# Kernel optimization log

Measured on AMD Instinct MI355X. Metric: run time of the kernel, lower is better.

The kernel has to match this reference:

```python
import jax, jax.numpy as jnp
import numpy as np

# DCRNN (PEMS-BAY scale) constants
N = 325      # num_nodes
B = 64       # batch_size
T = 12       # encoder seq_len
HZ = 12      # decoder horizon
U = 64       # rnn_units
DIN = 2      # input_dim
DOUT = 1     # output_dim
K = 2        # max_diffusion_step
NM = K + 1   # num diffusion matrices (Chebyshev, single laplacian support)


def _glorot(key, shape):
    lim = float(np.sqrt(6.0 / (shape[0] + shape[1])))
    return jax.random.uniform(key, shape, jnp.float32, -lim, lim)


def setup_inputs() -> dict:
    key = jax.random.key(0)
    ks = jax.random.split(key, 8)
    # random symmetric adjacency -> scaled Laplacian support (lambda_max ~= 2 approx)
    a = np.asarray(jax.random.uniform(ks[0], (N, N)))
    a = (a + a.T) * 0.5
    a = a * (a > 0.9)
    d = a.sum(1)
    dinv = 1.0 / np.sqrt(np.maximum(d, 1e-8))
    L = np.eye(N, dtype=np.float32) - (dinv[:, None] * a * dinv[None, :]).astype(np.float32)
    support = jnp.asarray(L - np.eye(N, dtype=np.float32))  # 2L/lambda_max - I with lambda_max=2

    def cell_params(k, din):
        f = (din + U) * NM
        k1, k2 = jax.random.split(k)
        return dict(gate_W=_glorot(k1, (f, 2 * U)), gate_b=jnp.zeros((2 * U,), jnp.float32),
                    cand_W=_glorot(k2, (f, U)), cand_b=jnp.zeros((U,), jnp.float32))

    inp = {"inputs": jax.random.normal(ks[1], (T, B, N * DIN), jnp.float32),
           "support": support}
    for name, din, kk in [("enc0", DIN, ks[2]), ("enc1", U, ks[3]),
                          ("dec0", DOUT, ks[4]), ("dec1", U, ks[5])]:
        for pn, v in cell_params(kk, din).items():
            inp[f"{name}_{pn}"] = v
    inp["proj_W"] = _glorot(ks[6], (U, DOUT))
    inp["proj_b"] = jnp.zeros((DOUT,), jnp.float32)
    return inp


def _gconv(x, support, W, b):
    # x: (B, N, F). Chebyshev diffusion: x0=x, x1=Lx, x2=2Lx1-x0, ...
    xs = [x]
    x0, x1 = x, jnp.einsum('mn,bnf->bmf', support, x)
    xs.append(x1)
    for _ in range(2, K + 1):
        x2 = 2.0 * jnp.einsum('mn,bnf->bmf', support, x1) - x0
        xs.append(x2)
        x0, x1 = x1, x2
    xk = jnp.concatenate(xs, axis=-1)  # (B, N, NM*F)
    return xk @ W + b


def _gru_cell(x, h, support, gW, gb, cW, cb):
    # diffusion-conv GRU: r,u gates then candidate
    ru = jax.nn.sigmoid(_gconv(jnp.concatenate([x, h], -1), support, gW, gb))
    r, u = jnp.split(ru, 2, axis=-1)
    c = jnp.tanh(_gconv(jnp.concatenate([x, r * h], -1), support, cW, cb))
    return u * h + (1.0 - u) * c


def reference(inputs, support,
              enc0_gate_W, enc0_gate_b, enc0_cand_W, enc0_cand_b,
              enc1_gate_W, enc1_gate_b, enc1_cand_W, enc1_cand_b,
              dec0_gate_W, dec0_gate_b, dec0_cand_W, dec0_cand_b,
              dec1_gate_W, dec1_gate_b, dec1_cand_W, dec1_cand_b,
              proj_W, proj_b):
    x_seq = inputs.reshape(T, B, N, DIN)
    h0 = jnp.zeros((B, N, U), inputs.dtype)

    def enc_step(carry, x):
        h_l0, h_l1 = carry
        h_l0 = _gru_cell(x, h_l0, support, enc0_gate_W, enc0_gate_b, enc0_cand_W, enc0_cand_b)
        h_l1 = _gru_cell(h_l0, h_l1, support, enc1_gate_W, enc1_gate_b, enc1_cand_W, enc1_cand_b)
        return (h_l0, h_l1), None

    (h_l0, h_l1), _ = jax.lax.scan(enc_step, (h0, h0), x_seq)

    def dec_step(carry, _):
        d_in, hd0, hd1 = carry
        hd0 = _gru_cell(d_in, hd0, support, dec0_gate_W, dec0_gate_b, dec0_cand_W, dec0_cand_b)
        hd1 = _gru_cell(hd0, hd1, support, dec1_gate_W, dec1_gate_b, dec1_cand_W, dec1_cand_b)
        out = hd1 @ proj_W + proj_b  # (B, N, DOUT)
        return (out, hd0, hd1), out.reshape(B, N * DOUT)

    start = jnp.zeros((B, N, DOUT), inputs.dtype)  # GO symbol
    _, outputs = jax.lax.scan(dec_step, (start, h_l0, h_l1), None, length=HZ)
    return outputs  # (horizon, B, N*DOUT)
```

## Files before the change

### kernel.cpp

```cpp
#include <hip/hip_runtime.h>

constexpr int N  = 325;
constexpr int B  = 64;
constexpr int T  = 12;
constexpr int HZ = 12;
constexpr int U  = 64;
constexpr int BN = B * N;

constexpr int SSTIL = 42;
constexpr int SSKC  = 11;
constexpr int XST   = 364;

typedef __attribute__((ext_vector_type(8))) short short8;
typedef __attribute__((ext_vector_type(4))) float floatx4;

__device__ inline unsigned short f2bf(float f) {
    unsigned u = __float_as_uint(f);
    u += 0x7fff + ((u >> 16) & 1);
    return (unsigned short)(u >> 16);
}
__device__ inline unsigned pack_hilo(float v) {
    const unsigned short hi = f2bf(v);
    const float hif = __uint_as_float(((unsigned)hi) << 16);
    const unsigned short lo = f2bf(v - hif);
    return (unsigned)hi | ((unsigned)lo << 16);
}
__device__ inline void unpack8(const uint4 u0, const uint4 u1,
                               short8& h, short8& l) {
    const unsigned uu[8] = {u0.x, u0.y, u0.z, u0.w, u1.x, u1.y, u1.z, u1.w};
    #pragma unroll
    for (int j = 0; j < 8; ++j) {
        h[j] = (short)(uu[j] & 0xffffu);
        l[j] = (short)(uu[j] >> 16);
    }
}


__global__ void zero_kernel(unsigned* __restrict__ p, long n) {
    long i = (long)blockIdx.x * blockDim.x + threadIdx.x;
    const long stride = (long)gridDim.x * blockDim.x;
    for (; i < n; i += stride) p[i] = 0u;
}

__global__ __launch_bounds__(256)
void s2_build(const float* __restrict__ S, float* __restrict__ S2)
{
    const int m = blockIdx.x;
    __shared__ float srow[N];
    for (int i = threadIdx.x; i < N; i += 256) srow[i] = S[m * N + i];
    __syncthreads();
    for (int c = threadIdx.x; c < N; c += 256) {
        float a = 0.f;
        for (int k = 0; k < N; ++k) a += srow[k] * S[k * N + c];
        S2[m * N + c] = a;
    }
}

__global__ __launch_bounds__(64)
void prepack_ss(const float* __restrict__ S, const float* __restrict__ S2,
                short* __restrict__ ssh, short* __restrict__ ssl)
{
    const int t = blockIdx.x, kc = blockIdx.y, lane = threadIdx.x;
    const int quad = lane >> 4, l15 = lane & 15;
    short8 hv, lv;
    #pragma unroll
    for (int j = 0; j < 8; ++j) {
        const int m = t * 16 + l15;
        const int k = kc * 32 + quad * 8 + j;
        float v = 0.f;
        if (k < N) {
            if (m < N) v = S[m * N + k];
            else if (m >= 336 && m < 336 + N) v = S2[(m - 336) * N + k];
        }
        const unsigned short hb = f2bf(v);
        hv[j] = (short)hb;
        lv[j] = (short)f2bf(v - __uint_as_float(((unsigned)hb) << 16));
    }
    const size_t off = ((size_t)(t * SSKC + kc) * 64 + lane);
    ((short8*)ssh)[off] = hv;
    ((short8*)ssl)[off] = lv;
}

__global__ __launch_bounds__(64)
void prepack_w(const float* __restrict__ W, short* __restrict__ Wh,
               short* __restrict__ Wl, int F, int Nout, int NT, int Z0KC)
{
    const int kc = blockIdx.x, n = blockIdx.y, lane = threadIdx.x;
    const int quad = lane >> 4, l15 = lane & 15;
    short8 hv, lv;
    #pragma unroll
    for (int j = 0; j < 8; ++j) {
        const int p   = kc * 32 + quad * 8 + j;
        const int col = n * 16 + l15;
        float w = 0.f;
        if (p < Z0KC * 32) {
            const int f = p;
            if (f < F)
                w = W[(size_t)f * Nout + col] - W[(size_t)(2 * F + f) * Nout + col];
        } else {
            const int q = p - Z0KC * 32;
            if (q < F)
                w = W[(size_t)(F + q) * Nout + col];
            else if (q < 2 * F)
                w = 2.f * W[(size_t)(2 * F + (q - F)) * Nout + col];
        }
        const unsigned short hb = f2bf(w);
        hv[j] = (short)hb;
        lv[j] = (short)f2bf(w - __uint_as_float(((unsigned)hb) << 16));
    }
    const size_t off = ((size_t)(kc * NT + n) * 64 + lane);
    ((short8*)Wh)[off] = hv;
    ((short8*)Wl)[off] = lv;
}

template<int DIN, int F, bool RM, bool ZV>
__device__ __forceinline__ void z0_frag(const float* __restrict__ x,
    const float* __restrict__ h, const float* __restrict__ ru,
    int row, int kc, int quad, short8& ah, short8& al)
{
    float v[8];
    if constexpr (ZV) {
        const int k0 = kc * 32 + quad * 8;
        if (k0 < 64) {
            const float4 a = *(const float4*)&x[(size_t)row * 64 + k0];
            const float4 b = *(const float4*)&x[(size_t)row * 64 + k0 + 4];
            v[0]=a.x; v[1]=a.y; v[2]=a.z; v[3]=a.w;
            v[4]=b.x; v[5]=b.y; v[6]=b.z; v[7]=b.w;
        } else {
            const int kk = k0 - 64;
            float4 a = *(const float4*)&h[(size_t)row * 64 + kk];
            float4 b = *(const float4*)&h[(size_t)row * 64 + kk + 4];
            if constexpr (RM) {
                const float4 ra = *(const float4*)&ru[(size_t)row * 128 + kk];
                const float4 rb = *(const float4*)&ru[(size_t)row * 128 + kk + 4];
                a.x *= ra.x; a.y *= ra.y; a.z *= ra.z; a.w *= ra.w;
                b.x *= rb.x; b.y *= rb.y; b.z *= rb.z; b.w *= rb.w;
            }
            v[0]=a.x; v[1]=a.y; v[2]=a.z; v[3]=a.w;
            v[4]=b.x; v[5]=b.y; v[6]=b.z; v[7]=b.w;
        }
    } else {
        #pragma unroll
        for (int j = 0; j < 8; ++j) {
            const int k = kc * 32 + quad * 8 + j;
            float t = 0.f;
            if (k < DIN) t = x[(size_t)row * DIN + k];
            else if (k < F) {
                t = h[(size_t)row * 64 + (k - DIN)];
                if constexpr (RM) t *= ru[(size_t)row * 128 + (k - DIN)];
            }
            v[j] = t;
        }
    }
    #pragma unroll
    for (int j = 0; j < 8; ++j) {
        const unsigned u = pack_hilo(v[j]);
        ah[j] = (short)(u & 0xffffu);
        al[j] = (short)(u >> 16);
    }
}

template<int DIN, int F, int YP, bool RMUL, bool VEC>
__device__ __forceinline__ void diffuse_body(
    const short8* __restrict__ ssh, const short8* __restrict__ ssl,
    const float* __restrict__ x, const float* __restrict__ h,
    const float* __restrict__ ru, unsigned* __restrict__ zcat,
    int cx, int b, unsigned* __restrict__ xls)
{
    const int c0 = cx * 32;
    const int tid = threadIdx.x, wave = tid >> 6, lane = tid & 63;
    const int quad = lane >> 4, l15 = lane & 15;

    if constexpr (VEC) {
        for (int idx4 = tid; idx4 < 352 * 8; idx4 += 896) {
            const int n = idx4 >> 3, f = (idx4 & 7) * 4, gf = c0 + f;
            uint4 pk = make_uint4(0u, 0u, 0u, 0u);
            if (n < N) {
                const int row = b * N + n;
                float4 v;
                if (gf < DIN) {
                    v = *(const float4*)&x[(size_t)row * DIN + gf];
                } else {
                    v = *(const float4*)&h[(size_t)row * U + (gf - DIN)];
                    if (RMUL) {
                        const float4 rv = *(const float4*)&ru[(size_t)row * 128 + (gf - DIN)];
                        v.x *= rv.x; v.y *= rv.y; v.z *= rv.z; v.w *= rv.w;
                    }
                }
                pk.x = pack_hilo(v.x); pk.y = pack_hilo(v.y);
                pk.z = pack_hilo(v.z); pk.w = pack_hilo(v.w);
            }
            xls[(f + 0) * XST + n] = pk.x;
            xls[(f + 1) * XST + n] = pk.y;
            xls[(f + 2) * XST + n] = pk.z;
            xls[(f + 3) * XST + n] = pk.w;
        }
    } else {
        for (int idx = tid; idx < 352 * 32; idx += 896) {
            const int n = idx >> 5, f = idx & 31, gf = c0 + f;
            unsigned u = 0u;
            if (n < N && gf < F) {
                const int row = b * N + n;
                float v;
                if (gf < DIN) {
                    v = x[(size_t)row * DIN + gf];
                } else {
                    v = h[(size_t)row * U + (gf - DIN)];
                    if (RMUL) v *= ru[(size_t)row * 128 + (gf - DIN)];
                }
                u = pack_hilo(v);
            }
            xls[f * XST + n] = u;
        }
    }
    __syncthreads();

    const int tb = wave * 3;

    floatx4 acc[3][2];
    #pragma unroll
    for (int i = 0; i < 3; ++i)
        #pragma unroll
        for (int n = 0; n < 2; ++n)
            acc[i][n] = (floatx4){0.f, 0.f, 0.f, 0.f};

    short8 cah[3], cal[3], nah[3], nal[3];
    #pragma unroll
    for (int i = 0; i < 3; ++i) {
        const size_t fo = (size_t)((tb + i) * SSKC) * 64 + lane;
        cah[i] = ssh[fo]; cal[i] = ssl[fo];
    }
    for (int kc = 0; kc < SSKC; ++kc) {
        if (kc + 1 < SSKC) {
            #pragma unroll
            for (int i = 0; i < 3; ++i) {
                const size_t fo = (size_t)((tb + i) * SSKC + kc + 1) * 64 + lane;
                nah[i] = ssh[fo]; nal[i] = ssl[fo];
            }
        }
        short8 bh[2], bl[2];
        const int koff = kc * 32 + quad * 8;
        #pragma unroll
        for (int n = 0; n < 2; ++n) {
            const uint4 u0 = *(const uint4*)&xls[(n * 16 + l15) * XST + koff];
            const uint4 u1 = *(const uint4*)&xls[(n * 16 + l15) * XST + koff + 4];
            unpack8(u0, u1, bh[n], bl[n]);
        }
        #pragma unroll
        for (int i = 0; i < 3; ++i)
            #pragma unroll
            for (int n = 0; n < 2; ++n) {
                acc[i][n] = __builtin_amdgcn_mfma_f32_16x16x32_bf16(cah[i], bh[n], acc[i][n], 0, 0, 0);
                acc[i][n] = __builtin_amdgcn_mfma_f32_16x16x32_bf16(cah[i], bl[n], acc[i][n], 0, 0, 0);
                acc[i][n] = __builtin_amdgcn_mfma_f32_16x16x32_bf16(cal[i], bh[n], acc[i][n], 0, 0, 0);
            }
        if (kc + 1 < SSKC) {
            #pragma unroll
            for (int i = 0; i < 3; ++i) { cah[i] = nah[i]; cal[i] = nal[i]; }
        }
    }

    #pragma unroll
    for (int i = 0; i < 3; ++i) {
        const int t = tb + i;
        #pragma unroll
        for (int n = 0; n < 2; ++n) {
            const int col = c0 + n * 16 + l15;
            if (col >= F) continue;
            #pragma unroll
            for (int r = 0; r < 4; ++r) {
                const int m = t * 16 + quad * 4 + r;
                if (m < N)
                    zcat[(size_t)(b * N + m) * YP + col] = pack_hilo(acc[i][n][r]);
                else if (m >= 336 && m < 336 + N)
                    zcat[(size_t)(b * N + (m - 336)) * YP + F + col] = pack_hilo(acc[i][n][r]);
            }
        }
    }
}


template<int DIN, int F, int Z0KC, int YKC, bool ZV>
__device__ __forceinline__ void gate_body(const unsigned* __restrict__ zcat,
    const float* __restrict__ x, const float* __restrict__ h,
    const short8* __restrict__ Wh, const short8* __restrict__ Wl,
    const float* __restrict__ bias, float* __restrict__ ruout, int bx, int nb)
{
    constexpr int YP = YKC * 32, NT = 4;
    const int tid = threadIdx.x, wave = tid >> 6, lane = tid & 63;
    const int quad = lane >> 4, l15 = lane & 15;
    const int row0 = bx * 64 + wave * 16;
    const int row = row0 + l15;

    floatx4 acc[NT];
    #pragma unroll
    for (int n = 0; n < NT; ++n) {
        const float bv = bias[(nb + n) * 16 + l15];
        acc[n] = (floatx4){bv, bv, bv, bv};
    }
    for (int kc = 0; kc < Z0KC; ++kc) {
        short8 ahi, alo;
        z0_frag<DIN, F, false, ZV>(x, h, nullptr, row, kc, quad, ahi, alo);
        const short8* __restrict__ wh = Wh + (size_t)(kc * 8 + nb) * 64 + lane;
        const short8* __restrict__ wl = Wl + (size_t)(kc * 8 + nb) * 64 + lane;
        #pragma unroll
        for (int n = 0; n < NT; ++n) {
            const short8 bh = wh[n * 64], bl = wl[n * 64];
            acc[n] = __builtin_amdgcn_mfma_f32_16x16x32_bf16(ahi, bh, acc[n], 0, 0, 0);
            acc[n] = __builtin_amdgcn_mfma_f32_16x16x32_bf16(ahi, bl, acc[n], 0, 0, 0);
            acc[n] = __builtin_amdgcn_mfma_f32_16x16x32_bf16(alo, bh, acc[n], 0, 0, 0);
        }
    }
    const unsigned* __restrict__ zrow = zcat + (size_t)row * YP + quad * 8;
    for (int kc = 0; kc < YKC; ++kc) {
        const uint4* p = (const uint4*)(zrow + kc * 32);
        short8 ahi, alo;
        unpack8(p[0], p[1], ahi, alo);
        const short8* __restrict__ wh = Wh + (size_t)((Z0KC + kc) * 8 + nb) * 64 + lane;
        const short8* __restrict__ wl = Wl + (size_t)((Z0KC + kc) * 8 + nb) * 64 + lane;
        #pragma unroll
        for (int n = 0; n < NT; ++n) {
            const short8 bh = wh[n * 64], bl = wl[n * 64];
            acc[n] = __builtin_amdgcn_mfma_f32_16x16x32_bf16(ahi, bh, acc[n], 0, 0, 0);
            acc[n] = __builtin_amdgcn_mfma_f32_16x16x32_bf16(ahi, bl, acc[n], 0, 0, 0);
            acc[n] = __builtin_amdgcn_mfma_f32_16x16x32_bf16(alo, bh, acc[n], 0, 0, 0);
        }
    }
    #pragma unroll
    for (int n = 0; n < NT; ++n) {
        const int col = (nb + n) * 16 + l15;
        #pragma unroll
        for (int r = 0; r < 4; ++r) {
            const int rw = row0 + quad * 4 + r;
            ruout[(size_t)rw * 128 + col] = 1.f / (1.f + __expf(-acc[n][r]));
        }
    }
}

template<int DIN, int F, int Z0KC, int YKC, bool ZV>
__device__ __forceinline__ void cand_body(const unsigned* __restrict__ zcat,
    const float* __restrict__ x, const float* __restrict__ h,
    const float* __restrict__ ru, const short8* __restrict__ Wh,
    const short8* __restrict__ Wl, const float* __restrict__ bias,
    float* __restrict__ hout, int bx, int nb)
{
    constexpr int YP = YKC * 32, NT = 2;
    const int tid = threadIdx.x, wave = tid >> 6, lane = tid & 63;
    const int quad = lane >> 4, l15 = lane & 15;
    const int row0 = bx * 64 + wave * 16;
    const int row = row0 + l15;

    floatx4 acc[NT];
    #pragma unroll
    for (int n = 0; n < NT; ++n) {
        const float bv = bias[(nb + n) * 16 + l15];
        acc[n] = (floatx4){bv, bv, bv, bv};
    }
    for (int kc = 0; kc < Z0KC; ++kc) {
        short8 ahi, alo;
        z0_frag<DIN, F, true, ZV>(x, h, ru, row, kc, quad, ahi, alo);
        const short8* __restrict__ wh = Wh + (size_t)(kc * 4 + nb) * 64 + lane;
        const short8* __restrict__ wl = Wl + (size_t)(kc * 4 + nb) * 64 + lane;
        #pragma unroll
        for (int n = 0; n < NT; ++n) {
            const short8 bh = wh[n * 64], bl = wl[n * 64];
            acc[n] = __builtin_amdgcn_mfma_f32_16x16x32_bf16(ahi, bh, acc[n], 0, 0, 0);
            acc[n] = __builtin_amdgcn_mfma_f32_16x16x32_bf16(ahi, bl, acc[n], 0, 0, 0);
            acc[n] = __builtin_amdgcn_mfma_f32_16x16x32_bf16(alo, bh, acc[n], 0, 0, 0);
        }
    }
    const unsigned* __restrict__ zrow = zcat + (size_t)row * YP + quad * 8;
    for (int kc = 0; kc < YKC; ++kc) {
        const uint4* p = (const uint4*)(zrow + kc * 32);
        short8 ahi, alo;
        unpack8(p[0], p[1], ahi, alo);
        const short8* __restrict__ wh = Wh + (size_t)((Z0KC + kc) * 4 + nb) * 64 + lane;
        const short8* __restrict__ wl = Wl + (size_t)((Z0KC + kc) * 4 + nb) * 64 + lane;
        #pragma unroll
        for (int n = 0; n < NT; ++n) {
            const short8 bh = wh[n * 64], bl = wl[n * 64];
            acc[n] = __builtin_amdgcn_mfma_f32_16x16x32_bf16(ahi, bh, acc[n], 0, 0, 0);
            acc[n] = __builtin_amdgcn_mfma_f32_16x16x32_bf16(ahi, bl, acc[n], 0, 0, 0);
            acc[n] = __builtin_amdgcn_mfma_f32_16x16x32_bf16(alo, bh, acc[n], 0, 0, 0);
        }
    }
    #pragma unroll
    for (int n = 0; n < NT; ++n) {
        const int col = (nb + n) * 16 + l15;
        #pragma unroll
        for (int r = 0; r < 4; ++r) {
            const int rw = row0 + quad * 4 + r;
            const float c  = tanhf(acc[n][r]);
            const float ug = ru[(size_t)rw * 128 + 64 + col];
            const float hv = h[(size_t)rw * 64 + col];
            hout[(size_t)rw * 64 + col] = ug * hv + (1.f - ug) * c;
        }
    }
}


template<int DIN, int F, int YP, bool RMUL, int CB, bool VEC>
__global__ __launch_bounds__(896, 7)
void diffuse_solo(const short8* __restrict__ ssh, const short8* __restrict__ ssl,
                  const float* __restrict__ x, const float* __restrict__ h,
                  const float* __restrict__ ru, unsigned* __restrict__ zcat)
{
    __shared__ __align__(16) unsigned xls[32 * XST];
    diffuse_body<DIN, F, YP, RMUL, VEC>(ssh, ssl, x, h, ru, zcat,
                                        CB + blockIdx.x, blockIdx.y, xls);
}

template<int DIN, int F, int Z0KC, int YKC, bool ZV>
__global__ __launch_bounds__(256)
void gate_cell(const unsigned* __restrict__ zcat, const float* __restrict__ x,
               const float* __restrict__ h, const short8* __restrict__ Wh,
               const short8* __restrict__ Wl, const float* __restrict__ bias,
               float* __restrict__ ru)
{
    gate_body<DIN, F, Z0KC, YKC, ZV>(zcat, x, h, Wh, Wl, bias, ru,
                                     blockIdx.x, blockIdx.y * 4);
}

template<int DIN, int F, int Z0KC, int YKC, bool ZV>
__global__ __launch_bounds__(256)
void cand_cell(const unsigned* __restrict__ zcat, const float* __restrict__ x,
               const float* __restrict__ h, const float* __restrict__ ru,
               const short8* __restrict__ Wh, const short8* __restrict__ Wl,
               const float* __restrict__ bias, float* __restrict__ hout)
{
    cand_body<DIN, F, Z0KC, YKC, ZV>(zcat, x, h, ru, Wh, Wl, bias, hout,
                                     blockIdx.x, blockIdx.y * 2);
}

__global__ __launch_bounds__(256)
void cand_proj(const unsigned* __restrict__ zcat, const float* __restrict__ x,
               const float* __restrict__ h, const float* __restrict__ ru,
               const short8* __restrict__ Wh, const short8* __restrict__ Wl,
               const float* __restrict__ bias, float* __restrict__ hout,
               const float* __restrict__ pW, const float* __restrict__ pb,
               float* __restrict__ outp, float* __restrict__ dec_in)
{
    constexpr int Z0KC = 4, YKC = 8, YP = 256, NT = 4;
    const int tid = threadIdx.x, wave = tid >> 6, lane = tid & 63;
    const int quad = lane >> 4, l15 = lane & 15;
    const int row0 = blockIdx.x * 64 + wave * 16;
    const int row = row0 + l15;

    floatx4 acc[NT];
    #pragma unroll
    for (int n = 0; n < NT; ++n) {
        const float bv = bias[n * 16 + l15];
        acc[n] = (floatx4){bv, bv, bv, bv};
    }
    for (int kc = 0; kc < Z0KC; ++kc) {
        short8 ahi, alo;
        z0_frag<64, 128, true, true>(x, h, ru, row, kc, quad, ahi, alo);
        const short8* __restrict__ wh = Wh + (size_t)(kc * 4) * 64 + lane;
        const short8* __restrict__ wl = Wl + (size_t)(kc * 4) * 64 + lane;
        #pragma unroll
        for (int n = 0; n < NT; ++n) {
            const short8 bh = wh[n * 64], bl = wl[n * 64];
            acc[n] = __builtin_amdgcn_mfma_f32_16x16x32_bf16(ahi, bh, acc[n], 0, 0, 0);
            acc[n] = __builtin_amdgcn_mfma_f32_16x16x32_bf16(ahi, bl, acc[n], 0, 0, 0);
            acc[n] = __builtin_amdgcn_mfma_f32_16x16x32_bf16(alo, bh, acc[n], 0, 0, 0);
        }
    }
    const unsigned* __restrict__ zrow = zcat + (size_t)row * YP + quad * 8;
    for (int kc = 0; kc < YKC; ++kc) {
        const uint4* p = (const uint4*)(zrow + kc * 32);
        short8 ahi, alo;
        unpack8(p[0], p[1], ahi, alo);
        const short8* __restrict__ wh = Wh + (size_t)((Z0KC + kc) * 4) * 64 + lane;
        const short8* __restrict__ wl = Wl + (size_t)((Z0KC + kc) * 4) * 64 + lane;
        #pragma unroll
        for (int n = 0; n < NT; ++n) {
            const short8 bh = wh[n * 64], bl = wl[n * 64];
            acc[n] = __builtin_amdgcn_mfma_f32_16x16x32_bf16(ahi, bh, acc[n], 0, 0, 0);
            acc[n] = __builtin_amdgcn_mfma_f32_16x16x32_bf16(ahi, bl, acc[n], 0, 0, 0);
            acc[n] = __builtin_amdgcn_mfma_f32_16x16x32_bf16(alo, bh, acc[n], 0, 0, 0);
        }
    }
    float pr[4] = {0.f, 0.f, 0.f, 0.f};
    #pragma unroll
    for (int n = 0; n < NT; ++n) {
        const int col = n * 16 + l15;
        const float pw = pW[col];
        #pragma unroll
        for (int r = 0; r < 4; ++r) {
            const int rw = row0 + quad * 4 + r;
            const float c  = tanhf(acc[n][r]);
            const float ug = ru[(size_t)rw * 128 + 64 + col];
            const float hv = h[(size_t)rw * 64 + col];
            const float hn = ug * hv + (1.f - ug) * c;
            hout[(size_t)rw * 64 + col] = hn;
            pr[r] += hn * pw;
        }
    }
    #pragma unroll
    for (int r = 0; r < 4; ++r) {
        float v = pr[r];
        v += __shfl_xor(v, 1); v += __shfl_xor(v, 2);
        v += __shfl_xor(v, 4); v += __shfl_xor(v, 8);
        if (l15 == 0) {
            const int rw = row0 + quad * 4 + r;
            const float o = v + pb[0];
            outp[rw]   = o;
            dec_in[rw] = o;
        }
    }
}


struct DuoDP {
    const short8 *ssh, *ssl;
    const float *xA, *hA, *ruA; unsigned* zA;
    const float *xB, *hB, *ruB; unsigned* zB;
    int cA, cbB;
};

template<bool RM>
__global__ __launch_bounds__(896, 7)
void diffuse_duo(DuoDP P)
{
    __shared__ __align__(16) unsigned xls[32 * XST];
    if ((int)blockIdx.x < P.cA)
        diffuse_body<2, 66, 160, RM, false>(P.ssh, P.ssl, P.xA, P.hA, P.ruA,
                                            P.zA, blockIdx.x, blockIdx.y, xls);
    else
        diffuse_body<64, 128, 256, RM, true>(P.ssh, P.ssl, P.xB, P.hB, P.ruB,
                                             P.zB, P.cbB + blockIdx.x - P.cA,
                                             blockIdx.y, xls);
}

struct DuoGP {
    const unsigned* zA; const float *xA, *hA;
    const short8 *WhA, *WlA; const float* bA; float* ruA;
    const unsigned* zB; const float *xB, *hB;
    const short8 *WhB, *WlB; const float* bB; float* ruB;
};

__global__ __launch_bounds__(256)
void gate_duo(DuoGP P)
{
    if (blockIdx.z == 0)
        gate_body<2, 66, 3, 5, false>(P.zA, P.xA, P.hA, P.WhA, P.WlA, P.bA,
                                      P.ruA, blockIdx.x, blockIdx.y * 4);
    else
        gate_body<64, 128, 4, 8, true>(P.zB, P.xB, P.hB, P.WhB, P.WlB, P.bB,
                                       P.ruB, blockIdx.x, blockIdx.y * 4);
}

struct DuoCP {
    const unsigned* zA; const float *xA, *hA, *ruA;
    const short8 *WhA, *WlA; const float* bA; float* hoA;
    const unsigned* zB; const float *xB, *hB, *ruB;
    const short8 *WhB, *WlB; const float* bB; float* hoB;
};

__global__ __launch_bounds__(256)
void cand_duo(DuoCP P)
{
    if (blockIdx.z == 0)
        cand_body<2, 66, 3, 5, false>(P.zA, P.xA, P.hA, P.ruA, P.WhA, P.WlA,
                                      P.bA, P.hoA, blockIdx.x, blockIdx.y * 2);
    else
        cand_body<64, 128, 4, 8, true>(P.zB, P.xB, P.hB, P.ruB, P.WhB, P.WlB,
                                       P.bB, P.hoB, blockIdx.x, blockIdx.y * 2);
}


extern "C" void kernel_launch(void* const* d_in, const int* in_sizes, int n_in,
                              void* d_out, int out_size, void* d_ws, size_t ws_size,
                              hipStream_t stream)
{
    const float* inputs = (const float*)d_in[0];
    const float* S      = (const float*)d_in[1];
    const float* Wt[4][4];
    for (int l = 0; l < 4; ++l)
        for (int j = 0; j < 4; ++j)
            Wt[l][j] = (const float*)d_in[2 + l * 4 + j];
    const float* pW = (const float*)d_in[18];
    const float* pb = (const float*)d_in[19];
    float* out = (float*)d_out;

    float*    ws     = (float*)d_ws;
    float*    H0[2]  = {ws, ws + (size_t)BN * U};
    float*    H1[2]  = {ws + 2 * (size_t)BN * U, ws + 3 * (size_t)BN * U};
    float*    dec_in = ws + 4 * (size_t)BN * U;
    float*    ruA    = dec_in + BN;
    float*    ruB    = ruA + (size_t)BN * 128;
    unsigned* zcatA  = (unsigned*)(ruB + (size_t)BN * 128);
    unsigned* zcatB  = zcatA + (size_t)BN * 160;
    float*    S2     = (float*)(zcatB + (size_t)BN * 256);
    char*     pp     = (char*)(S2 + (size_t)N * N);
    pp = (char*)(((uintptr_t)pp + 15) & ~(uintptr_t)15);

    short* ssh = (short*)pp;
    short* ssl = ssh + (size_t)SSTIL * SSKC * 64 * 8;
    char*  wpbase = (char*)(ssl + (size_t)SSTIL * SSKC * 64 * 8);

    const int Fs[4]   = {66, 128, 65, 128};
    const int KPs[4]  = {256, 384, 256, 384};
    const int Z0s[4]  = {3, 4, 3, 4};
    short *Wgh[4], *Wgl[4], *Wch[4], *Wcl[4];
    size_t off = 0;
    for (int l = 0; l < 4; ++l) {
        const size_t ge = (size_t)KPs[l] * 128, ce = (size_t)KPs[l] * 64;
        Wgh[l] = (short*)(wpbase + off); off += ge * 2;
        Wgl[l] = (short*)(wpbase + off); off += ge * 2;
        Wch[l] = (short*)(wpbase + off); off += ce * 2;
        Wcl[l] = (short*)(wpbase + off); off += ce * 2;
    }

    const long zn = (long)BN * (4 * U) + BN + (long)BN * 256 + (long)BN * (160 + 256);
    zero_kernel<<<2048, 256, 0, stream>>>((unsigned*)ws, zn);

    s2_build<<<N, 256, 0, stream>>>(S, S2);
    prepack_ss<<<dim3(SSTIL, SSKC), 64, 0, stream>>>(S, S2, ssh, ssl);
    for (int l = 0; l < 4; ++l) {
        prepack_w<<<dim3(KPs[l] / 32, 8), 64, 0, stream>>>(Wt[l][0], Wgh[l], Wgl[l],
                                                           Fs[l], 128, 8, Z0s[l]);
        prepack_w<<<dim3(KPs[l] / 32, 4), 64, 0, stream>>>(Wt[l][2], Wch[l], Wcl[l],
                                                           Fs[l], 64, 4, Z0s[l]);
    }

    const short8* SSH = (const short8*)ssh;
    const short8* SSL = (const short8*)ssl;
    int p0 = 0, p1 = 0;

    for (int s = 0; s <= T; ++s) {
        const float* x0 = inputs + (size_t)s * BN * 2;
        const bool a = (s < T), b1 = (s >= 1);
        if (a && b1) {
            DuoDP dp{SSH, SSL, x0, H0[p0], nullptr, zcatA,
                     H0[p0], H1[p1], nullptr, zcatB, 3, 0};
            diffuse_duo<false><<<dim3(7, B), 896, 0, stream>>>(dp);
            DuoGP gp{zcatA, x0, H0[p0], (short8*)Wgh[0], (short8*)Wgl[0], Wt[0][1], ruA,
                     zcatB, H0[p0], H1[p1], (short8*)Wgh[1], (short8*)Wgl[1], Wt[1][1], ruB};
            gate_duo<<<dim3(BN / 64, 2, 2), 256, 0, stream>>>(gp);
            DuoDP dp2{SSH, SSL, x0, H0[p0], ruA, zcatA,
                      H0[p0], H1[p1], ruB, zcatB, 3, 2};
            diffuse_duo<true><<<dim3(5, B), 896, 0, stream>>>(dp2);
            DuoCP cp{zcatA, x0, H0[p0], ruA, (short8*)Wch[0], (short8*)Wcl[0], Wt[0][3], H0[p0 ^ 1],
                     zcatB, H0[p0], H1[p1], ruB, (short8*)Wch[1], (short8*)Wcl[1], Wt[1][3], H1[p1 ^ 1]};
            cand_duo<<<dim3(BN / 64, 2, 2), 256, 0, stream>>>(cp);
            p0 ^= 1; p1 ^= 1;
        } else if (a) {
            diffuse_solo<2, 66, 160, false, 0, false><<<dim3(3, B), 896, 0, stream>>>(
                SSH, SSL, x0, H0[p0], nullptr, zcatA);
            gate_cell<2, 66, 3, 5, false><<<dim3(BN / 64, 2), 256, 0, stream>>>(
                zcatA, x0, H0[p0], (short8*)Wgh[0], (short8*)Wgl[0], Wt[0][1], ruA);
            diffuse_solo<2, 66, 160, true, 0, false><<<dim3(3, B), 896, 0, stream>>>(
                SSH, SSL, x0, H0[p0], ruA, zcatA);
            cand_cell<2, 66, 3, 5, false><<<dim3(BN / 64, 2), 256, 0, stream>>>(
                zcatA, x0, H0[p0], ruA, (short8*)Wch[0], (short8*)Wcl[0], Wt[0][3], H0[p0 ^ 1]);
            p0 ^= 1;
        } else {
            diffuse_solo<64, 128, 256, false, 0, true><<<dim3(4, B), 896, 0, stream>>>(
                SSH, SSL, H0[p0], H1[p1], nullptr, zcatB);
            gate_cell<64, 128, 4, 8, true><<<dim3(BN / 64, 2), 256, 0, stream>>>(
                zcatB, H0[p0], H1[p1], (short8*)Wgh[1], (short8*)Wgl[1], Wt[1][1], ruB);
            diffuse_solo<64, 128, 256, true, 2, true><<<dim3(2, B), 896, 0, stream>>>(
                SSH, SSL, H0[p0], H1[p1], ruB, zcatB);
            cand_cell<64, 128, 4, 8, true><<<dim3(BN / 64, 2), 256, 0, stream>>>(
                zcatB, H0[p0], H1[p1], ruB, (short8*)Wch[1], (short8*)Wcl[1], Wt[1][3], H1[p1 ^ 1]);
            p1 ^= 1;
        }
    }

    for (int hz = 0; hz < HZ; ++hz) {
        diffuse_solo<1, 65, 160, false, 0, false><<<dim3(3, B), 896, 0, stream>>>(
            SSH, SSL, dec_in, H0[p0], nullptr, zcatB);
        gate_cell<1, 65, 3, 5, false><<<dim3(BN / 64, 2), 256, 0, stream>>>(
            zcatB, dec_in, H0[p0], (short8*)Wgh[2], (short8*)Wgl[2], Wt[2][1], ruA);
        diffuse_solo<1, 65, 160, true, 0, false><<<dim3(3, B), 896, 0, stream>>>(
            SSH, SSL, dec_in, H0[p0], ruA, zcatB);
        cand_cell<1, 65, 3, 5, false><<<dim3(BN / 64, 2), 256, 0, stream>>>(
            zcatB, dec_in, H0[p0], ruA, (short8*)Wch[2], (short8*)Wcl[2], Wt[2][3], H0[p0 ^ 1]);
        p0 ^= 1;
        diffuse_solo<64, 128, 256, false, 0, true><<<dim3(4, B), 896, 0, stream>>>(
            SSH, SSL, H0[p0], H1[p1], nullptr, zcatB);
        gate_cell<64, 128, 4, 8, true><<<dim3(BN / 64, 2), 256, 0, stream>>>(
            zcatB, H0[p0], H1[p1], (short8*)Wgh[3], (short8*)Wgl[3], Wt[3][1], ruA);
        diffuse_solo<64, 128, 256, true, 2, true><<<dim3(2, B), 896, 0, stream>>>(
            SSH, SSL, H0[p0], H1[p1], ruA, zcatB);
        cand_proj<<<BN / 64, 256, 0, stream>>>(
            zcatB, H0[p0], H1[p1], ruA, (short8*)Wch[3], (short8*)Wcl[3], Wt[3][3],
            H1[p1 ^ 1], pW, pb, out + (size_t)hz * BN, dec_in);
        p1 ^= 1;
    }
}
```

Measured before the change: 3.964 ms.

## Skip re-diffusing r-independent columns and co-launch decoder layer-1 hidden diffusion

The diffusion kernels now take an absolute column offset instead of a chunk index. The candidate-pass diffusion then only covers the hidden-state columns that depend on the reset gate, reusing the input-column diffusion already written by the gate pass. In the decoder, the layer-1 hidden-state diffusion, which does not depend on the new layer-0 state, is merged into one launch with the layer-0 gate diffusion. Layer 0 moves to its own zcat buffer so the two can share that launch, and the later layer-1 diffusion shrinks to the layer-0-output columns. This removes redundant diffusion work and some launches, but it relies on zcat entries staying valid across kernels and on unaligned column offsets in the scalar path.

```diff
diff --git a/kernel.cpp b/kernel.cpp
--- a/kernel.cpp
+++ b/kernel.cpp
@@ -165,9 +165,8 @@
     const short8* __restrict__ ssh, const short8* __restrict__ ssl,
     const float* __restrict__ x, const float* __restrict__ h,
     const float* __restrict__ ru, unsigned* __restrict__ zcat,
-    int cx, int b, unsigned* __restrict__ xls)
-{
-    const int c0 = cx * 32;
+    int c0, int b, unsigned* __restrict__ xls)
+{
     const int tid = threadIdx.x, wave = tid >> 6, lane = tid & 63;
     const int quad = lane >> 4, l15 = lane & 15;
 
@@ -399,7 +398,7 @@
 }
 
 
-template<int DIN, int F, int YP, bool RMUL, int CB, bool VEC>
+template<int DIN, int F, int YP, bool RMUL, int C0OFF, bool VEC>
 __global__ __launch_bounds__(896, 7)
 void diffuse_solo(const short8* __restrict__ ssh, const short8* __restrict__ ssl,
                   const float* __restrict__ x, const float* __restrict__ h,
@@ -407,7 +406,7 @@
 {
     __shared__ __align__(16) unsigned xls[32 * XST];
     diffuse_body<DIN, F, YP, RMUL, VEC>(ssh, ssl, x, h, ru, zcat,
-                                        CB + blockIdx.x, blockIdx.y, xls);
+                                        C0OFF + blockIdx.x * 32, blockIdx.y, xls);
 }
 
 template<int DIN, int F, int Z0KC, int YKC, bool ZV>
@@ -515,7 +514,9 @@
     const short8 *ssh, *ssl;
     const float *xA, *hA, *ruA; unsigned* zA;
     const float *xB, *hB, *ruB; unsigned* zB;
-    int cA, cbB;
+    int cA;
+    int coA;
+    int coB;
 };
 
 template<bool RM>
@@ -525,11 +526,28 @@
     __shared__ __align__(16) unsigned xls[32 * XST];
     if ((int)blockIdx.x < P.cA)
         diffuse_body<2, 66, 160, RM, false>(P.ssh, P.ssl, P.xA, P.hA, P.ruA,
-                                            P.zA, blockIdx.x, blockIdx.y, xls);
+                                            P.zA, P.coA + blockIdx.x * 32,
+                                            blockIdx.y, xls);
     else
         diffuse_body<64, 128, 256, RM, true>(P.ssh, P.ssl, P.xB, P.hB, P.ruB,
-                                             P.zB, P.cbB + blockIdx.x - P.cA,
+                                             P.zB,
+                                             P.coB + (blockIdx.x - P.cA) * 32,
                                              blockIdx.y, xls);
+}
+
+__global__ __launch_bounds__(896, 7)
+void diffuse_duo_dec(DuoDP P)
+{
+    __shared__ __align__(16) unsigned xls[32 * XST];
+    if ((int)blockIdx.x < P.cA)
+        diffuse_body<1, 65, 160, false, false>(P.ssh, P.ssl, P.xA, P.hA, nullptr,
+                                               P.zA, P.coA + blockIdx.x * 32,
+                                               blockIdx.y, xls);
+    else
+        diffuse_body<64, 128, 256, false, true>(P.ssh, P.ssl, P.xB, P.hB, nullptr,
+                                                P.zB,
+                                                P.coB + (blockIdx.x - P.cA) * 32,
+                                                blockIdx.y, xls);
 }
 
 struct DuoGP {
@@ -633,14 +651,14 @@
         const bool a = (s < T), b1 = (s >= 1);
         if (a && b1) {
             DuoDP dp{SSH, SSL, x0, H0[p0], nullptr, zcatA,
-                     H0[p0], H1[p1], nullptr, zcatB, 3, 0};
+                     H0[p0], H1[p1], nullptr, zcatB, 3, 0, 0};
             diffuse_duo<false><<<dim3(7, B), 896, 0, stream>>>(dp);
             DuoGP gp{zcatA, x0, H0[p0], (short8*)Wgh[0], (short8*)Wgl[0], Wt[0][1], ruA,
                      zcatB, H0[p0], H1[p1], (short8*)Wgh[1], (short8*)Wgl[1], Wt[1][1], ruB};
             gate_duo<<<dim3(BN / 64, 2, 2), 256, 0, stream>>>(gp);
             DuoDP dp2{SSH, SSL, x0, H0[p0], ruA, zcatA,
-                      H0[p0], H1[p1], ruB, zcatB, 3, 2};
-            diffuse_duo<true><<<dim3(5, B), 896, 0, stream>>>(dp2);
+                      H0[p0], H1[p1], ruB, zcatB, 2, 2, 64};
+            diffuse_duo<true><<<dim3(4, B), 896, 0, stream>>>(dp2);
             DuoCP cp{zcatA, x0, H0[p0], ruA, (short8*)Wch[0], (short8*)Wcl[0], Wt[0][3], H0[p0 ^ 1],
                      zcatB, H0[p0], H1[p1], ruB, (short8*)Wch[1], (short8*)Wcl[1], Wt[1][3], H1[p1 ^ 1]};
             cand_duo<<<dim3(BN / 64, 2, 2), 256, 0, stream>>>(cp);
@@ -650,7 +668,7 @@
                 SSH, SSL, x0, H0[p0], nullptr, zcatA);
             gate_cell<2, 66, 3, 5, false><<<dim3(BN / 64, 2), 256, 0, stream>>>(
                 zcatA, x0, H0[p0], (short8*)Wgh[0], (short8*)Wgl[0], Wt[0][1], ruA);
-            diffuse_solo<2, 66, 160, true, 0, false><<<dim3(3, B), 896, 0, stream>>>(
+            diffuse_solo<2, 66, 160, true, 2, false><<<dim3(2, B), 896, 0, stream>>>(
                 SSH, SSL, x0, H0[p0], ruA, zcatA);
             cand_cell<2, 66, 3, 5, false><<<dim3(BN / 64, 2), 256, 0, stream>>>(
                 zcatA, x0, H0[p0], ruA, (short8*)Wch[0], (short8*)Wcl[0], Wt[0][3], H0[p0 ^ 1]);
@@ -660,7 +678,7 @@
                 SSH, SSL, H0[p0], H1[p1], nullptr, zcatB);
             gate_cell<64, 128, 4, 8, true><<<dim3(BN / 64, 2), 256, 0, stream>>>(
                 zcatB, H0[p0], H1[p1], (short8*)Wgh[1], (short8*)Wgl[1], Wt[1][1], ruB);
-            diffuse_solo<64, 128, 256, true, 2, true><<<dim3(2, B), 896, 0, stream>>>(
+            diffuse_solo<64, 128, 256, true, 64, true><<<dim3(2, B), 896, 0, stream>>>(
                 SSH, SSL, H0[p0], H1[p1], ruB, zcatB);
             cand_cell<64, 128, 4, 8, true><<<dim3(BN / 64, 2), 256, 0, stream>>>(
                 zcatB, H0[p0], H1[p1], ruB, (short8*)Wch[1], (short8*)Wcl[1], Wt[1][3], H1[p1 ^ 1]);
@@ -669,20 +687,21 @@
     }
 
     for (int hz = 0; hz < HZ; ++hz) {
-        diffuse_solo<1, 65, 160, false, 0, false><<<dim3(3, B), 896, 0, stream>>>(
-            SSH, SSL, dec_in, H0[p0], nullptr, zcatB);
+        DuoDP dd{SSH, SSL, dec_in, H0[p0], nullptr, zcatA,
+                 H0[p0], H1[p1], nullptr, zcatB, 3, 0, 64};
+        diffuse_duo_dec<<<dim3(5, B), 896, 0, stream>>>(dd);
         gate_cell<1, 65, 3, 5, false><<<dim3(BN / 64, 2), 256, 0, stream>>>(
-            zcatB, dec_in, H0[p0], (short8*)Wgh[2], (short8*)Wgl[2], Wt[2][1], ruA);
-        diffuse_solo<1, 65, 160, true, 0, false><<<dim3(3, B), 896, 0, stream>>>(
-            SSH, SSL, dec_in, H0[p0], ruA, zcatB);
+            zcatA, dec_in, H0[p0], (short8*)Wgh[2], (short8*)Wgl[2], Wt[2][1], ruA);
+        diffuse_solo<1, 65, 160, true, 1, false><<<dim3(2, B), 896, 0, stream>>>(
+            SSH, SSL, dec_in, H0[p0], ruA, zcatA);
         cand_cell<1, 65, 3, 5, false><<<dim3(BN / 64, 2), 256, 0, stream>>>(
-            zcatB, dec_in, H0[p0], ruA, (short8*)Wch[2], (short8*)Wcl[2], Wt[2][3], H0[p0 ^ 1]);
+            zcatA, dec_in, H0[p0], ruA, (short8*)Wch[2], (short8*)Wcl[2], Wt[2][3], H0[p0 ^ 1]);
         p0 ^= 1;
-        diffuse_solo<64, 128, 256, false, 0, true><<<dim3(4, B), 896, 0, stream>>>(
+        diffuse_solo<64, 128, 256, false, 0, true><<<dim3(2, B), 896, 0, stream>>>(
             SSH, SSL, H0[p0], H1[p1], nullptr, zcatB);
         gate_cell<64, 128, 4, 8, true><<<dim3(BN / 64, 2), 256, 0, stream>>>(
             zcatB, H0[p0], H1[p1], (short8*)Wgh[3], (short8*)Wgl[3], Wt[3][1], ruA);
-        diffuse_solo<64, 128, 256, true, 2, true><<<dim3(2, B), 896, 0, stream>>>(
+        diffuse_solo<64, 128, 256, true, 64, true><<<dim3(2, B), 896, 0, stream>>>(
             SSH, SSL, H0[p0], H1[p1], ruA, zcatB);
         cand_proj<<<BN / 64, 256, 0, stream>>>(
             zcatB, H0[p0], H1[p1], ruA, (short8*)Wch[3], (short8*)Wcl[3], Wt[3][3],
```

Result: no change. 3.990 ms (+0.7%).
